# Performance work log

Hardware: AMD Instinct MI355X
Metric: run time of the kernel (lower is better)

The kernel has to match this reference:

```python
import jax, jax.numpy as jnp
import numpy as np

SCALE = 2
PAD = 4
EPS = 1e-5
K = 5
N, C, H, W = 4, 64, 128, 128


def _splits(a, s):
    # (..., W, H) -> (..., W/s, H/s, s*s), block decimation matching torch view/permute
    *lead, Wd, Hd = a.shape
    b = a.reshape(*lead, s, Wd // s, s, Hd // s)
    nl = len(lead)
    b = jnp.transpose(b, tuple(range(nl)) + (nl + 1, nl + 3, nl, nl + 2))
    return b.reshape(*lead, Wd // s, Hd // s, s * s)


def _p2o(psf, Hs, Ws):
    # PSF -> OTF: zero-pad, roll to center at origin, FFT
    kh, kw = psf.shape[-2], psf.shape[-1]
    otf = jnp.zeros(psf.shape[:-2] + (Hs, Ws), psf.dtype).at[..., :kh, :kw].set(psf)
    otf = jnp.roll(otf, (-(kh // 2), -(kw // 2)), axis=(-2, -1))
    return jnp.fft.fftn(otf, axes=(-2, -1))


def _upsample(x, s):
    # s-fold zero-filling upsampler (S^T y)
    n, c, h, w = x.shape
    return jnp.zeros((n, c, h * s, w * s), x.dtype).at[..., ::s, ::s].set(x)


def setup_inputs() -> dict:
    key = jax.random.key(0)
    kx, kw_, _ = jax.random.split(key, 3)
    x = jax.random.normal(kx, (N, C, H, W), dtype=jnp.float32)
    w_raw = jax.random.normal(kw_, (1, C, K, K), dtype=jnp.float32)
    weight = jax.nn.softmax(w_raw.reshape(1, C, -1), axis=-1).reshape(1, C, K, K)
    bias = jnp.zeros((1, C, 1, 1), dtype=jnp.float32)
    return {"x": x, "weight": weight, "bias": bias}


def reference(x, weight, bias):
    s = SCALE
    xp = jnp.pad(x, ((0, 0), (0, 0), (PAD, PAD), (PAD, PAD)), mode="wrap")  # circular
    biaseps = jax.nn.sigmoid(bias - 9.0) + EPS  # (1,C,1,1)
    _, _, h, w = xp.shape
    STy = _upsample(xp, s)  # zero-filled upsample
    # nearest-neighbor interpolate by integer factor s
    xn = jnp.repeat(jnp.repeat(xp, s, axis=-2), s, axis=-1)
    FB = _p2o(weight, h * s, w * s)           # (1,C,hs,ws) complex
    FBC = jnp.conj(FB)
    F2B = jnp.abs(FB) ** 2                     # real
    FBFy = FBC * jnp.fft.fftn(STy, axes=(-2, -1))
    FR = FBFy + jnp.fft.fftn(biaseps * xn, axes=(-2, -1))
    x1 = FB * FR
    FBR = jnp.mean(_splits(x1, s), axis=-1)    # (N,C,h,w) complex
    invW = jnp.mean(_splits(F2B, s), axis=-1)  # (1,C,h,w) real
    invWBR = FBR / (invW + biaseps)
    FCBinvWBR = FBC * jnp.tile(invWBR, (1, 1, s, s))
    FX = (FR - FCBinvWBR) / biaseps
    out = jnp.real(jnp.fft.ifftn(FX, axes=(-2, -1)))
    out = out[..., PAD * s:-PAD * s, PAD * s:-PAD * s]
    return out
```

## Files before the change

kernel.cpp:

```cpp
#include <hip/hip_runtime.h>
#include <math.h>


#define MDIM 136
#define RSCF 146
#define RSC4 73
#define HC   69
#define PLANE_HALF (MDIM*HC)
#define NPLANES 256
#define LDS_BYTES (MDIM*RSC4*16 + 306*8)
#define PI_D 3.14159265358979323846
#define NTH 1024

__device__ __forceinline__ int slot136(int k) { return 17*(k & 7) + (k >> 3); }
__device__ __forceinline__ int slot68(int k)  { return 17*(k & 3) + (k >> 2); }

__device__ __forceinline__ float4 q_add(float4 a, float4 b)
{ return make_float4(a.x+b.x, a.y+b.y, a.z+b.z, a.w+b.w); }
__device__ __forceinline__ float4 q_sub(float4 a, float4 b)
{ return make_float4(a.x-b.x, a.y-b.y, a.z-b.z, a.w-b.w); }
__device__ __forceinline__ float4 q_muli(float4 a, float d)
{ return make_float4(-d*a.y, d*a.x, -d*a.w, d*a.z); }
__device__ __forceinline__ float4 q_scale(float4 a, float s)
{ return make_float4(s*a.x, s*a.y, s*a.z, s*a.w); }
__device__ __forceinline__ float4 q_fma(float4 a, float s, float4 acc)
{ return make_float4(fmaf(a.x,s,acc.x), fmaf(a.y,s,acc.y),
                     fmaf(a.z,s,acc.z), fmaf(a.w,s,acc.w)); }
__device__ __forceinline__ float4 cmul4(float4 q, float2 w)
{ return make_float4(q.x*w.x - q.y*w.y, q.x*w.y + q.y*w.x,
                     q.z*w.x - q.w*w.y, q.z*w.y + q.w*w.x); }

template<int DIR, class F>
__device__ __forceinline__ void dft17_sink(float2* z, int base, int stride, F f)
{
    constexpr float C17[9] = {1.f, 0.93247223f, 0.73900892f, 0.44573836f,
                              0.09226836f, -0.27366299f, -0.60263464f,
                              -0.85021714f, -0.98297310f};
    constexpr float S17[9] = {0.f, 0.36124167f, 0.67369564f, 0.89516329f,
                              0.99573418f, 0.96182564f, 0.79801723f,
                              0.52643216f, 0.18374952f};
    constexpr float d = (DIR > 0) ? 1.f : -1.f;
    float xr[17], xi[17];
#pragma unroll
    for (int n = 0; n < 17; n++) {
        float2 v = z[base + n*stride];
        xr[n] = v.x; xi[n] = v.y;
    }
    float ar[8], ai[8], br[8], bi[8];
#pragma unroll
    for (int n = 1; n <= 8; n++) {
        ar[n-1] = xr[n] + xr[17-n];  ai[n-1] = xi[n] + xi[17-n];
        br[n-1] = xr[n] - xr[17-n];  bi[n-1] = xi[n] - xi[17-n];
    }
    float s0r = xr[0], s0i = xi[0];
#pragma unroll
    for (int n = 0; n < 8; n++) { s0r += ar[n]; s0i += ai[n]; }
    f(0, s0r, s0i);
#pragma unroll
    for (int k = 1; k <= 8; k++) {
        float Pr = xr[0], Pi = xi[0], Qr = 0.f, Qi = 0.f;
#pragma unroll
        for (int n = 1; n <= 8; n++) {
            int m = (k*n) % 17;
            float cc = (m <= 8) ? C17[m] : C17[17-m];
            float ss = (m <= 8) ? S17[m] : -S17[17-m];
            Pr = fmaf(ar[n-1], cc, Pr);
            Pi = fmaf(ai[n-1], cc, Pi);
            Qr = fmaf(br[n-1], ss, Qr);
            Qi = fmaf(bi[n-1], ss, Qi);
        }
        f(k,    Pr - d*Qi, Pi + d*Qr);
        f(17-k, Pr + d*Qi, Pi - d*Qr);
    }
}

template<int DIR>
__device__ __forceinline__ void radix4_tw(float2* z, const float2* t68, int base, int n2,
                                          float2 Z0, float2 Z1, float2 Z2, float2 Z3)
{
    constexpr float d = (DIR > 0) ? 1.0f : -1.0f;
    float t0r = Z0.x+Z2.x, t0i = Z0.y+Z2.y;
    float t1r = Z0.x-Z2.x, t1i = Z0.y-Z2.y;
    float t2r = Z1.x+Z3.x, t2i = Z1.y+Z3.y;
    float t3r = Z1.x-Z3.x, t3i = Z1.y-Z3.y;
    float X0r = t0r+t2r,     X0i = t0i+t2i;
    float X2r = t0r-t2r,     X2i = t0i-t2i;
    float X1r = t1r - d*t3i, X1i = t1i + d*t3r;
    float X3r = t1r + d*t3i, X3i = t1i - d*t3r;
    z[base + n2] = make_float2(X0r, X0i);
    float2 w1 = t68[n2], w2 = t68[17 + n2], w3 = t68[34 + n2];
    if (DIR < 0) { w1.y = -w1.y; w2.y = -w2.y; w3.y = -w3.y; }
    z[base + 17 + n2] = make_float2(X1r*w1.x - X1i*w1.y, X1r*w1.y + X1i*w1.x);
    z[base + 34 + n2] = make_float2(X2r*w2.x - X2i*w2.y, X2r*w2.y + X2i*w2.x);
    z[base + 51 + n2] = make_float2(X3r*w3.x - X3i*w3.y, X3r*w3.y + X3i*w3.x);
}

template<int DIR>
__device__ __forceinline__ void radix4q_tw(float4* z, const float2* t68, int base, int n2,
                                           float4 Z0, float4 Z1, float4 Z2, float4 Z3)
{
    constexpr float d = (DIR > 0) ? 1.0f : -1.0f;
    float4 t0 = q_add(Z0, Z2), t1 = q_sub(Z0, Z2);
    float4 t2 = q_add(Z1, Z3), t3 = q_sub(Z1, Z3);
    float4 X0 = q_add(t0, t2), X2 = q_sub(t0, t2);
    float4 it3 = q_muli(t3, d);
    float4 X1 = q_add(t1, it3), X3 = q_sub(t1, it3);
    z[base + n2] = X0;
    float2 w1 = t68[n2], w2 = t68[17 + n2], w3 = t68[34 + n2];
    z[base + 17 + n2] = cmul4(X1, w1);
    z[base + 34 + n2] = cmul4(X2, w2);
    z[base + 51 + n2] = cmul4(X3, w3);
}

template<int DIR>
__device__ __forceinline__ void fft136_s1_body(float2* z, const float2* t136,
                                               int c, int n2)
{
    constexpr float d = (DIR > 0) ? 1.0f : -1.0f;
    constexpr float C707 = 0.70710678118654752f;
    float xr[8], xi[8];
#pragma unroll
    for (int n1 = 0; n1 < 8; n1++) {
        float2 v = z[(17*n1 + n2)*RSCF + c];
        xr[n1] = v.x; xi[n1] = v.y;
    }
    float e0r = xr[0]+xr[4], e0i = xi[0]+xi[4];
    float e1r = xr[0]-xr[4], e1i = xi[0]-xi[4];
    float o0r = xr[2]+xr[6], o0i = xi[2]+xi[6];
    float o1r = xr[2]-xr[6], o1i = xi[2]-xi[6];
    float E0r = e0r+o0r, E0i = e0i+o0i;
    float E2r = e0r-o0r, E2i = e0i-o0i;
    float E1r = e1r - d*o1i, E1i = e1i + d*o1r;
    float E3r = e1r + d*o1i, E3i = e1i - d*o1r;
    float f0r = xr[1]+xr[5], f0i = xi[1]+xi[5];
    float f1r = xr[1]-xr[5], f1i = xi[1]-xi[5];
    float h0r = xr[3]+xr[7], h0i = xi[3]+xi[7];
    float h1r = xr[3]-xr[7], h1i = xi[3]-xi[7];
    float O0r = f0r+h0r, O0i = f0i+h0i;
    float O2r = f0r-h0r, O2i = f0i-h0i;
    float O1r = f1r - d*h1i, O1i = f1i + d*h1r;
    float O3r = f1r + d*h1i, O3i = f1i - d*h1r;
    float t1r =  C707*(O1r - d*O1i), t1i = C707*(O1i + d*O1r);
    float t2r = -d*O2i,              t2i = d*O2r;
    float t3r = -C707*(O3r + d*O3i), t3i = C707*(d*O3r - O3i);
    float Xr[8], Xi[8];
    Xr[0]=E0r+O0r; Xi[0]=E0i+O0i;  Xr[4]=E0r-O0r; Xi[4]=E0i-O0i;
    Xr[1]=E1r+t1r; Xi[1]=E1i+t1i;  Xr[5]=E1r-t1r; Xi[5]=E1i-t1i;
    Xr[2]=E2r+t2r; Xi[2]=E2i+t2i;  Xr[6]=E2r-t2r; Xi[6]=E2i-t2i;
    Xr[3]=E3r+t3r; Xi[3]=E3i+t3i;  Xr[7]=E3r-t3r; Xi[7]=E3i-t3i;
    z[n2*RSCF + c] = make_float2(Xr[0], Xi[0]);
#pragma unroll
    for (int k1 = 1; k1 < 8; k1++) {
        float2 w = t136[(k1-1)*17 + n2];
        if (DIR < 0) w.y = -w.y;
        z[(17*k1 + n2)*RSCF + c] = make_float2(Xr[k1]*w.x - Xi[k1]*w.y,
                                               Xr[k1]*w.y + Xi[k1]*w.x);
    }
}

template<int DIR>
__device__ __forceinline__ void fft136q_s1_body(float4* z, const float2* t136,
                                                int c, int n2)
{
    constexpr float d = (DIR > 0) ? 1.0f : -1.0f;
    constexpr float C707 = 0.70710678118654752f;
    float4 x[8];
#pragma unroll
    for (int n1 = 0; n1 < 8; n1++) x[n1] = z[(17*n1 + n2)*RSC4 + c];
    float4 e0 = q_add(x[0], x[4]), e1 = q_sub(x[0], x[4]);
    float4 o0 = q_add(x[2], x[6]), o1 = q_sub(x[2], x[6]);
    float4 E0 = q_add(e0, o0), E2 = q_sub(e0, o0);
    float4 io1 = q_muli(o1, d);
    float4 E1 = q_add(e1, io1), E3 = q_sub(e1, io1);
    float4 f0 = q_add(x[1], x[5]), f1 = q_sub(x[1], x[5]);
    float4 h0 = q_add(x[3], x[7]), h1 = q_sub(x[3], x[7]);
    float4 O0 = q_add(f0, h0), O2 = q_sub(f0, h0);
    float4 ih1 = q_muli(h1, d);
    float4 O1 = q_add(f1, ih1), O3 = q_sub(f1, ih1);
    float4 t1 = q_scale(q_add(O1, q_muli(O1, d)), C707);
    float4 t2 = q_muli(O2, d);
    float4 t3 = q_scale(q_sub(O3, q_muli(O3, d)), -C707);
    float4 X0 = q_add(E0, O0), X4 = q_sub(E0, O0);
    float4 X1 = q_add(E1, t1), X5 = q_sub(E1, t1);
    float4 X2 = q_add(E2, t2), X6 = q_sub(E2, t2);
    float4 X3 = q_add(E3, t3), X7 = q_sub(E3, t3);
    z[n2*RSC4 + c] = X0;
    z[(17*1 + n2)*RSC4 + c] = cmul4(X1, t136[0*17 + n2]);
    z[(17*2 + n2)*RSC4 + c] = cmul4(X2, t136[1*17 + n2]);
    z[(17*3 + n2)*RSC4 + c] = cmul4(X3, t136[2*17 + n2]);
    z[(17*4 + n2)*RSC4 + c] = cmul4(X4, t136[3*17 + n2]);
    z[(17*5 + n2)*RSC4 + c] = cmul4(X5, t136[4*17 + n2]);
    z[(17*6 + n2)*RSC4 + c] = cmul4(X6, t136[5*17 + n2]);
    z[(17*7 + n2)*RSC4 + c] = cmul4(X7, t136[6*17 + n2]);
}

__device__ __forceinline__ float4 c2r_pack4(float4 a, float4 b, float2 w)
{
    float Sx = a.x + b.x, Sy = a.y - b.y;
    float Dx = a.x - b.x, Dy = a.y + b.y;
    float Ox = w.x*Dx - w.y*Dy, Oy = w.x*Dy + w.y*Dx;
    float Sz = a.z + b.z, Sw = a.w - b.w;
    float Dz = a.z - b.z, Dw = a.w + b.w;
    float Oz = w.x*Dz - w.y*Dw, Ow = w.x*Dw + w.y*Dz;
    return make_float4(Sx - Oy, Sy + Ox, Sz - Ow, Sw + Oz);
}

__global__ __launch_bounds__(1024, 4) void conv_kernel(const float* __restrict__ x,
                                                       const float4* __restrict__ Abuf,
                                                       float* __restrict__ out)
{
    extern __shared__ float4 z4s[];
    float4* z4    = z4s;
    float2* zf    = (float2*)z4s;
    float2* lutI  = (float2*)(z4s + MDIM*RSC4);
    float2* tI136 = lutI + MDIM;
    float2* tI68  = tI136 + 119;
    const int tid = threadIdx.x;
    const int nc  = blockIdx.x;
    const int c   = nc & 63;

    if (tid < MDIM) {
        float s, cc; sincosf(2.0f*(float)PI_D*(float)tid/136.0f, &s, &cc);
        lutI[tid] = make_float2(cc, s);
    } else if (tid < MDIM + 119) {
        int it = tid - MDIM;
        int k1 = it/17 + 1, n2 = it - (it/17)*17;
        float s, cc; sincosf((float)(PI_D/68.0)*(float)(k1*n2), &s, &cc);
        tI136[it] = make_float2(cc, s);
    } else if (tid < MDIM + 119 + 51) {
        int it = tid - MDIM - 119;
        int j = it/17, n2 = it - 17*j;
        float s, cc; sincosf((float)(PI_D/34.0)*(float)((j+1)*n2), &s, &cc);
        tI68[it] = make_float2(cc, s);
    }
    const float* xp = x + (size_t)nc * (128*128);
    {
        int i = tid / 68, n = tid - (tid/68)*68;
        for (int e = tid; e < MDIM*68; e += NTH) {
            int si = (i + 124) & 127;
            int j0 = (2*n + 124) & 127;
            zf[i*RSCF + n] = *reinterpret_cast<const float2*>(xp + si*128 + j0);
            i += 15; n += 4; if (n >= 68) { n -= 68; i++; }
        }
    }
    __syncthreads();
    {
        int row = tid / 17;
        int n2  = tid - row*17;
        for (int e = tid; e < MDIM*17; e += NTH) {
            int base = row*RSCF;
            float2 Z0 = zf[base + n2];
            float2 Z1 = zf[base + 17 + n2];
            float2 Z2 = zf[base + 34 + n2];
            float2 Z3 = zf[base + 51 + n2];
            radix4_tw<-1>(zf, tI68, base, n2, Z0, Z1, Z2, Z3);
            row += 60; n2 += 4; if (n2 >= 17) { n2 -= 17; row++; }
        }
    }
    __syncthreads();
    if (tid < MDIM*4) {
        int row = tid >> 2, k1 = tid & 3;
        int base = row*RSCF + 17*k1;
        dft17_sink<-1>(zf, base, 1, [&](int k2, float re, float im) {
            zf[base + k2] = make_float2(re, im);
        });
    }
    __syncthreads();
    {
        int row = tid / 35, k = tid - (tid/35)*35;
        for (int e = tid; e < MDIM*35; e += NTH) {
            int base = row*RSCF;
            int sa = slot68(k);
            float2 Za = zf[base+sa];
            float Zar = Za.x, Zai = Za.y;
            float Zbr, Zbi; int sb;
            if (k == 0) { Zbr = Zar; Zbi = Zai; sb = 68; }
            else {
                int kk = 68-k; sb = slot68(kk);
                float2 Zb = zf[base+sb]; Zbr = Zb.x; Zbi = Zb.y;
            }
            float2 w = lutI[k];
            float wc = w.x, ws = -w.y;
            float Er = 0.5f*(Zar + Zbr), Ei = 0.5f*(Zai - Zbi);
            float Dr = 0.5f*(Zar - Zbr), Di = 0.5f*(Zai + Zbi);
            float Tr = wc*Dr - ws*Di, Ti = wc*Di + ws*Dr;
            zf[base+sa] = make_float2(Er + Ti, Ei - Tr);
            float E2r = Er,  E2i = -Ei;
            float D2r = -Dr, D2i = Di;
            float w2c = -wc, w2s = ws;
            float T2r = w2c*D2r - w2s*D2i, T2i = w2c*D2i + w2s*D2r;
            zf[base+sb] = make_float2(E2r + T2i, E2i - T2r);
            row += 29; k += 9; if (k >= 35) { k -= 35; row++; }
        }
    }
    __syncthreads();
    for (int e = tid; e < HC*17; e += NTH) {
        int cc = (e*241) >> 12;
        int n2 = e - cc*17;
        fft136_s1_body<-1>(zf, tI136, cc, n2);
    }
    __syncthreads();
    if (tid < HC*8) {
        int cc = tid >> 3, k1 = tid & 7;
        int base = 17*k1*RSCF + cc;
        dft17_sink<-1>(zf, base, RSCF, [&](int k2, float re, float im) {
            zf[base + k2*RSCF] = make_float2(re, im);
        });
    }
    __syncthreads();
    float2 Xreg[10];
    {
        int g1 = tid / HC, g2 = tid - (tid/HC)*HC;
#pragma unroll
        for (int k = 0; k < 10; k++) {
            if (k < 9 || tid < PLANE_HALF - 9*NTH) {
                int cq = (g2 == 68) ? 68 : slot68(g2);
                Xreg[k] = zf[slot136(g1)*RSCF + cq];
            }
            g1 += 14; g2 += 58; if (g2 >= HC) { g2 -= HC; g1++; }
        }
    }
    __syncthreads();
    float* op = out + (size_t)nc * (256*256);
#pragma unroll 1
    for (int u = 0; u < 2; u++) {
        const float4* Ap = Abuf + (size_t)(c*2 + u) * PLANE_HALF;
        {
            int g1 = tid / HC, g2 = tid - (tid/HC)*HC;
#pragma unroll
            for (int k = 0; k < 10; k++) {
                if (k < 9 || tid < PLANE_HALF - 9*NTH) {
                    float2 xv = Xreg[k];
                    float4 av = Ap[tid + k*NTH];
                    z4[g1*RSC4 + g2] = make_float4(
                        av.x*xv.x - av.y*xv.y, av.x*xv.y + av.y*xv.x,
                        av.z*xv.x - av.w*xv.y, av.z*xv.y + av.w*xv.x);
                }
                g1 += 14; g2 += 58; if (g2 >= HC) { g2 -= HC; g1++; }
            }
        }
        __syncthreads();
        for (int e = tid; e < HC*17; e += NTH) {
            int cc = (e*241) >> 12;
            int n2 = e - cc*17;
            fft136q_s1_body<1>(z4, tI136, cc, n2);
        }
        __syncthreads();
        {
            float2* z2 = (float2*)z4;
            for (int it = tid; it < 2*HC*8; it += NTH) {
                int half = it & 1;
                int i  = it >> 1;
                int cc = i >> 3, k1 = i & 7;
                int base = 2*(17*k1*RSC4 + cc) + half;
                dft17_sink<1>(z2, base, 2*RSC4, [&](int k2, float re, float im) {
                    z2[base + k2*2*RSC4] = make_float2(re, im);
                });
            }
        }
        __syncthreads();
        for (int it = tid; it < MDIM*9; it += NTH) {
            int row = (it*7282) >> 16;
            int g   = it - row*9;
            int base = row*RSC4;
            if (g == 0) {
                float4 T0  = z4[base],    T17 = z4[base+17], T34 = z4[base+34],
                       T51 = z4[base+51], T68 = z4[base+68];
                float4 Z0 = c2r_pack4(T0,  T68, lutI[0]);
                float4 Z1 = c2r_pack4(T17, T51, lutI[17]);
                float4 Z2 = c2r_pack4(T34, T34, lutI[34]);
                float4 Z3 = c2r_pack4(T51, T17, lutI[51]);
                radix4q_tw<1>(z4, tI68, base, 0, Z0, Z1, Z2, Z3);
            } else {
                int gb = 17 - g;
                float4 Ta0 = z4[base+g],    Ta1 = z4[base+g+17],
                       Ta2 = z4[base+g+34], Ta3 = z4[base+g+51];
                float4 Tb0 = z4[base+gb],    Tb1 = z4[base+gb+17],
                       Tb2 = z4[base+gb+34], Tb3 = z4[base+gb+51];
                float4 Za0 = c2r_pack4(Ta0, Tb3, lutI[g]);
                float4 Za1 = c2r_pack4(Ta1, Tb2, lutI[g+17]);
                float4 Za2 = c2r_pack4(Ta2, Tb1, lutI[g+34]);
                float4 Za3 = c2r_pack4(Ta3, Tb0, lutI[g+51]);
                float4 Zb0 = c2r_pack4(Tb0, Ta3, lutI[gb]);
                float4 Zb1 = c2r_pack4(Tb1, Ta2, lutI[gb+17]);
                float4 Zb2 = c2r_pack4(Tb2, Ta1, lutI[gb+34]);
                float4 Zb3 = c2r_pack4(Tb3, Ta0, lutI[gb+51]);
                radix4q_tw<1>(z4, tI68, base, g,  Za0, Za1, Za2, Za3);
                radix4q_tw<1>(z4, tI68, base, gb, Zb0, Zb1, Zb2, Zb3);
            }
        }
        __syncthreads();
        {
            float2* z2 = (float2*)z4;
            for (int it = tid; it < 2*MDIM*4; it += NTH) {
                int half = it & 1;
                int i   = it >> 1;
                int row = i >> 2, k1 = i & 3;
                int base = 2*(row*RSC4 + 17*k1) + half;
                dft17_sink<1>(z2, base, 2, [&](int k2, float re, float im) {
                    z2[base + 2*k2] = make_float2(re, im);
                });
            }
        }
        __syncthreads();
        {
            int m  = 2 + (tid & 63);
            int y1 = 4 + (tid >> 6);
            int a  = slot136(y1)*RSC4 + slot68(m);
            float* rowp = op + (size_t)(2*y1 + u - 8)*256 + 4*m - 8;
#pragma unroll
            for (int it = 0; it < 8; ++it) {
                float4 w = z4[a];
                *reinterpret_cast<float4*>(rowp) = make_float4(w.x, w.z, w.y, w.w);
                a += 2*RSC4;
                rowp += 32*256;
            }
        }
        __syncthreads();
    }
}

__global__ void prep_kernel(const float* __restrict__ weight,
                            const float* __restrict__ bias,
                            float4* __restrict__ Abuf)
{
    __shared__ float tabc[272], tabs[272];
    __shared__ float Rs[69*5*4];
    for (int t = threadIdx.x; t < 272; t += blockDim.x) {
        float s, c; sincosf(-2.0f*(float)PI_D*(float)t/272.0f, &s, &c);
        tabc[t] = c; tabs[t] = s;
    }
    const int c     = blockIdx.x >> 3;
    const int chunk = blockIdx.x & 7;
    const float* wp = weight + c*25;
    const float r = 1.0f/(1.0f + expf(9.0f - bias[c])) + 1e-5f;
    __syncthreads();
    for (int it = threadIdx.x; it < 69*5; it += blockDim.x) {
        int g2 = it / 5, a = it - 5*g2;
        float c2 = tabc[g2], s2 = tabs[g2];
        float e2r[5], e2i[5];
        e2r[2]=1.0f; e2i[2]=0.0f; e2r[3]=c2; e2i[3]=s2;
        e2r[4]=c2*c2-s2*s2; e2i[4]=2.0f*c2*s2;
        e2r[1]=c2; e2i[1]=-s2; e2r[0]=e2r[4]; e2i[0]=-e2i[4];
        float w0=wp[a*5+0], w1=wp[a*5+1], w2=wp[a*5+2], w3=wp[a*5+3], w4=wp[a*5+4];
        float Rer = w0*e2r[0] + w2*e2r[2] + w4*e2r[4];
        float Rei = w0*e2i[0] + w2*e2i[2] + w4*e2i[4];
        float Ror = w1*e2r[1] + w3*e2r[3];
        float Roi = w1*e2i[1] + w3*e2i[3];
        Rs[it*4+0] = Rer + Ror;  Rs[it*4+1] = Rei + Roi;
        Rs[it*4+2] = Rer - Ror;  Rs[it*4+3] = Rei - Roi;
    }
    __syncthreads();

    const int e_lo = chunk * 1173;
    const int e_hi = e_lo + 1173;
    int e  = e_lo + (int)threadIdx.x;
    int g1 = e / HC, g2 = e - (e/HC)*HC;
    for (; e < e_hi; e += blockDim.x) {
        float c1 = tabc[g1], s1 = tabs[g1];
        float e1r[5], e1i[5];
        e1r[2]=1.0f; e1i[2]=0.0f; e1r[3]=c1; e1i[3]=s1;
        e1r[4]=c1*c1-s1*s1; e1i[4]=2.0f*c1*s1;
        e1r[1]=c1; e1i[1]=-s1; e1r[0]=e1r[4]; e1i[0]=-e1i[4];

        float FBr[2][2], FBi[2][2];
#pragma unroll
        for (int b1 = 0; b1 < 2; b1++) {
            float Per=0.f, Pei=0.f, Por=0.f, Poi=0.f;
#pragma unroll
            for (int a = 0; a < 5; a++) {
                float Rr = Rs[(g2*5+a)*4 + 2*b1];
                float Ri = Rs[(g2*5+a)*4 + 2*b1 + 1];
                float tr = e1r[a]*Rr - e1i[a]*Ri;
                float ti = e1r[a]*Ri + e1i[a]*Rr;
                if (a & 1) { Por += tr; Poi += ti; } else { Per += tr; Pei += ti; }
            }
            FBr[0][b1] = Per + Por;  FBi[0][b1] = Pei + Poi;
            FBr[1][b1] = Per - Por;  FBi[1][b1] = Pei - Poi;
        }
        float c2 = tabc[g2], s2 = tabs[g2];
        float ur[2]={1.0f+c1, 1.0f-c1}, ui[2]={s1, -s1};
        float vr[2]={1.0f+c2, 1.0f-c2}, vi[2]={s2, -s2};
        float Br_[2][2], Bi_[2][2];
#pragma unroll
        for (int a1 = 0; a1 < 2; a1++)
#pragma unroll
            for (int b1 = 0; b1 < 2; b1++) {
                Br_[a1][b1] = ur[a1]*vr[b1] - ui[a1]*vi[b1];
                Bi_[a1][b1] = ur[a1]*vi[b1] + ui[a1]*vr[b1];
            }
        float invW=0.f, Qr=0.f, Qi=0.f;
#pragma unroll
        for (int a1 = 0; a1 < 2; a1++)
#pragma unroll
            for (int b1 = 0; b1 < 2; b1++) {
                invW += FBr[a1][b1]*FBr[a1][b1] + FBi[a1][b1]*FBi[a1][b1];
                Qr += FBr[a1][b1]*Br_[a1][b1] - FBi[a1][b1]*Bi_[a1][b1];
                Qi += FBr[a1][b1]*Bi_[a1][b1] + FBi[a1][b1]*Br_[a1][b1];
            }
        invW *= 0.25f; Qr *= 0.25f; Qi *= 0.25f;
        float den = 1.0f/(invW + r);
        float Sr = (1.0f - Qr)*den, Si = -Qi*den;
        float Mr[2][2], Mi[2][2];
#pragma unroll
        for (int a1 = 0; a1 < 2; a1++)
#pragma unroll
            for (int b1 = 0; b1 < 2; b1++) {
                Mr[a1][b1] = Br_[a1][b1] + FBr[a1][b1]*Sr + FBi[a1][b1]*Si;
                Mi[a1][b1] = Bi_[a1][b1] + FBr[a1][b1]*Si - FBi[a1][b1]*Sr;
            }
        const float scale = 1.0f/73984.0f;
#pragma unroll
        for (int uu = 0; uu < 2; uu++) {
            float ov[4];
#pragma unroll
            for (int vv = 0; vv < 2; vv++) {
                float sr=0.f, si=0.f;
#pragma unroll
                for (int a1 = 0; a1 < 2; a1++)
#pragma unroll
                    for (int b1 = 0; b1 < 2; b1++) {
                        if ((a1*uu + b1*vv) & 1) { sr -= Mr[a1][b1]; si -= Mi[a1][b1]; }
                        else                     { sr += Mr[a1][b1]; si += Mi[a1][b1]; }
                    }
                int t = g1*uu + g2*vv;
                float pc = tabc[t], ps = -tabs[t];
                ov[2*vv]   = (pc*sr - ps*si)*scale;
                ov[2*vv+1] = (pc*si + ps*sr)*scale;
            }
            Abuf[((size_t)(c*2 + uu))*PLANE_HALF + e] =
                make_float4(ov[0], ov[1], ov[2], ov[3]);
        }
        g1 += 3; g2 += 49; if (g2 >= HC) { g2 -= HC; g1++; }
    }
}

extern "C" void kernel_launch(void* const* d_in, const int* in_sizes, int n_in,
                              void* d_out, int out_size, void* d_ws, size_t ws_size,
                              hipStream_t stream)
{
    const float* x      = (const float*)d_in[0];
    const float* weight = (const float*)d_in[1];
    const float* bias   = (const float*)d_in[2];
    float* out = (float*)d_out;

    float4* Abuf = (float4*)d_ws;

    (void)hipFuncSetAttribute((const void*)conv_kernel,
                              hipFuncAttributeMaxDynamicSharedMemorySize,
                              (int)LDS_BYTES);

    prep_kernel<<<512, 256, 0, stream>>>(weight, bias, Abuf);
    conv_kernel<<<NPLANES, 1024, LDS_BYTES, stream>>>(x, Abuf, out);
}
```

Before: 131.0 us.

## Process one output phase per inverse FFT pass to halve LDS footprint

The inverse-FFT loop now handles each of the four (u,v) output phases separately with float2 planes, where it used to handle two phases at once as float4. Twiddle and LUT tables move into the padding columns of the LDS matrix, so LDS per block shrinks to about half and launch bounds ask for higher occupancy. The cost is twice as many inverse-FFT passes, barriers and Abuf reads, plus scattered scalar output stores where the code used float4 stores.

```diff
diff --git a/kernel.cpp b/kernel.cpp
--- a/kernel.cpp
+++ b/kernel.cpp
@@ -3,32 +3,23 @@
 
 
 #define MDIM 136
-#define RSCF 146
-#define RSC4 73
+#define RSC2 73
 #define HC   69
 #define PLANE_HALF (MDIM*HC)
 #define NPLANES 256
-#define LDS_BYTES (MDIM*RSC4*16 + 306*8)
+#define LDS_BYTES (MDIM*RSC2*8)
 #define PI_D 3.14159265358979323846
 #define NTH 1024
 
 __device__ __forceinline__ int slot136(int k) { return 17*(k & 7) + (k >> 3); }
 __device__ __forceinline__ int slot68(int k)  { return 17*(k & 3) + (k >> 2); }
 
-__device__ __forceinline__ float4 q_add(float4 a, float4 b)
-{ return make_float4(a.x+b.x, a.y+b.y, a.z+b.z, a.w+b.w); }
-__device__ __forceinline__ float4 q_sub(float4 a, float4 b)
-{ return make_float4(a.x-b.x, a.y-b.y, a.z-b.z, a.w-b.w); }
-__device__ __forceinline__ float4 q_muli(float4 a, float d)
-{ return make_float4(-d*a.y, d*a.x, -d*a.w, d*a.z); }
-__device__ __forceinline__ float4 q_scale(float4 a, float s)
-{ return make_float4(s*a.x, s*a.y, s*a.z, s*a.w); }
-__device__ __forceinline__ float4 q_fma(float4 a, float s, float4 acc)
-{ return make_float4(fmaf(a.x,s,acc.x), fmaf(a.y,s,acc.y),
-                     fmaf(a.z,s,acc.z), fmaf(a.w,s,acc.w)); }
-__device__ __forceinline__ float4 cmul4(float4 q, float2 w)
-{ return make_float4(q.x*w.x - q.y*w.y, q.x*w.y + q.y*w.x,
-                     q.z*w.x - q.w*w.y, q.z*w.y + q.w*w.x); }
+__device__ __forceinline__ float2 LUTI(const float2* z, int t)
+{ return z[t*RSC2 + 69]; }
+__device__ __forceinline__ float2 T136(const float2* z, int i)
+{ return z[i*RSC2 + 70]; }
+__device__ __forceinline__ float2 T68v(const float2* z, int i)
+{ return z[i*RSC2 + 71]; }
 
 template<int DIR, class F>
 __device__ __forceinline__ void dft17_sink(float2* z, int base, int stride, F f)
@@ -75,7 +66,7 @@
 }
 
 template<int DIR>
-__device__ __forceinline__ void radix4_tw(float2* z, const float2* t68, int base, int n2,
+__device__ __forceinline__ void radix4_tw(float2* z, int base, int n2,
                                           float2 Z0, float2 Z1, float2 Z2, float2 Z3)
 {
     constexpr float d = (DIR > 0) ? 1.0f : -1.0f;
@@ -88,7 +79,7 @@
     float X1r = t1r - d*t3i, X1i = t1i + d*t3r;
     float X3r = t1r + d*t3i, X3i = t1i - d*t3r;
     z[base + n2] = make_float2(X0r, X0i);
-    float2 w1 = t68[n2], w2 = t68[17 + n2], w3 = t68[34 + n2];
+    float2 w1 = T68v(z, n2), w2 = T68v(z, 17 + n2), w3 = T68v(z, 34 + n2);
     if (DIR < 0) { w1.y = -w1.y; w2.y = -w2.y; w3.y = -w3.y; }
     z[base + 17 + n2] = make_float2(X1r*w1.x - X1i*w1.y, X1r*w1.y + X1i*w1.x);
     z[base + 34 + n2] = make_float2(X2r*w2.x - X2i*w2.y, X2r*w2.y + X2i*w2.x);
@@ -96,32 +87,14 @@
 }
 
 template<int DIR>
-__device__ __forceinline__ void radix4q_tw(float4* z, const float2* t68, int base, int n2,
-                                           float4 Z0, float4 Z1, float4 Z2, float4 Z3)
-{
-    constexpr float d = (DIR > 0) ? 1.0f : -1.0f;
-    float4 t0 = q_add(Z0, Z2), t1 = q_sub(Z0, Z2);
-    float4 t2 = q_add(Z1, Z3), t3 = q_sub(Z1, Z3);
-    float4 X0 = q_add(t0, t2), X2 = q_sub(t0, t2);
-    float4 it3 = q_muli(t3, d);
-    float4 X1 = q_add(t1, it3), X3 = q_sub(t1, it3);
-    z[base + n2] = X0;
-    float2 w1 = t68[n2], w2 = t68[17 + n2], w3 = t68[34 + n2];
-    z[base + 17 + n2] = cmul4(X1, w1);
-    z[base + 34 + n2] = cmul4(X2, w2);
-    z[base + 51 + n2] = cmul4(X3, w3);
-}
-
-template<int DIR>
-__device__ __forceinline__ void fft136_s1_body(float2* z, const float2* t136,
-                                               int c, int n2)
+__device__ __forceinline__ void fft136_s1_body(float2* z, int c, int n2)
 {
     constexpr float d = (DIR > 0) ? 1.0f : -1.0f;
     constexpr float C707 = 0.70710678118654752f;
     float xr[8], xi[8];
 #pragma unroll
     for (int n1 = 0; n1 < 8; n1++) {
-        float2 v = z[(17*n1 + n2)*RSCF + c];
+        float2 v = z[(17*n1 + n2)*RSC2 + c];
         xr[n1] = v.x; xi[n1] = v.y;
     }
     float e0r = xr[0]+xr[4], e0i = xi[0]+xi[4];
@@ -148,90 +121,46 @@
     Xr[1]=E1r+t1r; Xi[1]=E1i+t1i;  Xr[5]=E1r-t1r; Xi[5]=E1i-t1i;
     Xr[2]=E2r+t2r; Xi[2]=E2i+t2i;  Xr[6]=E2r-t2r; Xi[6]=E2i-t2i;
     Xr[3]=E3r+t3r; Xi[3]=E3i+t3i;  Xr[7]=E3r-t3r; Xi[7]=E3i-t3i;
-    z[n2*RSCF + c] = make_float2(Xr[0], Xi[0]);
+    z[n2*RSC2 + c] = make_float2(Xr[0], Xi[0]);
 #pragma unroll
     for (int k1 = 1; k1 < 8; k1++) {
-        float2 w = t136[(k1-1)*17 + n2];
+        float2 w = T136(z, (k1-1)*17 + n2);
         if (DIR < 0) w.y = -w.y;
-        z[(17*k1 + n2)*RSCF + c] = make_float2(Xr[k1]*w.x - Xi[k1]*w.y,
+        z[(17*k1 + n2)*RSC2 + c] = make_float2(Xr[k1]*w.x - Xi[k1]*w.y,
                                                Xr[k1]*w.y + Xi[k1]*w.x);
     }
 }
 
-template<int DIR>
-__device__ __forceinline__ void fft136q_s1_body(float4* z, const float2* t136,
-                                                int c, int n2)
-{
-    constexpr float d = (DIR > 0) ? 1.0f : -1.0f;
-    constexpr float C707 = 0.70710678118654752f;
-    float4 x[8];
-#pragma unroll
-    for (int n1 = 0; n1 < 8; n1++) x[n1] = z[(17*n1 + n2)*RSC4 + c];
-    float4 e0 = q_add(x[0], x[4]), e1 = q_sub(x[0], x[4]);
-    float4 o0 = q_add(x[2], x[6]), o1 = q_sub(x[2], x[6]);
-    float4 E0 = q_add(e0, o0), E2 = q_sub(e0, o0);
-    float4 io1 = q_muli(o1, d);
-    float4 E1 = q_add(e1, io1), E3 = q_sub(e1, io1);
-    float4 f0 = q_add(x[1], x[5]), f1 = q_sub(x[1], x[5]);
-    float4 h0 = q_add(x[3], x[7]), h1 = q_sub(x[3], x[7]);
-    float4 O0 = q_add(f0, h0), O2 = q_sub(f0, h0);
-    float4 ih1 = q_muli(h1, d);
-    float4 O1 = q_add(f1, ih1), O3 = q_sub(f1, ih1);
-    float4 t1 = q_scale(q_add(O1, q_muli(O1, d)), C707);
-    float4 t2 = q_muli(O2, d);
-    float4 t3 = q_scale(q_sub(O3, q_muli(O3, d)), -C707);
-    float4 X0 = q_add(E0, O0), X4 = q_sub(E0, O0);
-    float4 X1 = q_add(E1, t1), X5 = q_sub(E1, t1);
-    float4 X2 = q_add(E2, t2), X6 = q_sub(E2, t2);
-    float4 X3 = q_add(E3, t3), X7 = q_sub(E3, t3);
-    z[n2*RSC4 + c] = X0;
-    z[(17*1 + n2)*RSC4 + c] = cmul4(X1, t136[0*17 + n2]);
-    z[(17*2 + n2)*RSC4 + c] = cmul4(X2, t136[1*17 + n2]);
-    z[(17*3 + n2)*RSC4 + c] = cmul4(X3, t136[2*17 + n2]);
-    z[(17*4 + n2)*RSC4 + c] = cmul4(X4, t136[3*17 + n2]);
-    z[(17*5 + n2)*RSC4 + c] = cmul4(X5, t136[4*17 + n2]);
-    z[(17*6 + n2)*RSC4 + c] = cmul4(X6, t136[5*17 + n2]);
-    z[(17*7 + n2)*RSC4 + c] = cmul4(X7, t136[6*17 + n2]);
-}
-
-__device__ __forceinline__ float4 c2r_pack4(float4 a, float4 b, float2 w)
-{
-    float Sx = a.x + b.x, Sy = a.y - b.y;
-    float Dx = a.x - b.x, Dy = a.y + b.y;
-    float Ox = w.x*Dx - w.y*Dy, Oy = w.x*Dy + w.y*Dx;
-    float Sz = a.z + b.z, Sw = a.w - b.w;
-    float Dz = a.z - b.z, Dw = a.w + b.w;
-    float Oz = w.x*Dz - w.y*Dw, Ow = w.x*Dw + w.y*Dz;
-    return make_float4(Sx - Oy, Sy + Ox, Sz - Ow, Sw + Oz);
-}
-
-__global__ __launch_bounds__(1024, 4) void conv_kernel(const float* __restrict__ x,
-                                                       const float4* __restrict__ Abuf,
+__device__ __forceinline__ float2 c2r_pack(float2 a, float2 b, float2 w)
+{
+    float Sr = a.x + b.x, Si = a.y - b.y;
+    float Dr = a.x - b.x, Di = a.y + b.y;
+    float Or = w.x*Dr - w.y*Di, Oi = w.x*Di + w.y*Dr;
+    return make_float2(Sr - Oi, Si + Or);
+}
+
+__global__ __launch_bounds__(1024, 8) void conv_kernel(const float* __restrict__ x,
+                                                       const float2* __restrict__ Abuf,
                                                        float* __restrict__ out)
 {
-    extern __shared__ float4 z4s[];
-    float4* z4    = z4s;
-    float2* zf    = (float2*)z4s;
-    float2* lutI  = (float2*)(z4s + MDIM*RSC4);
-    float2* tI136 = lutI + MDIM;
-    float2* tI68  = tI136 + 119;
+    extern __shared__ float2 z2[];
     const int tid = threadIdx.x;
     const int nc  = blockIdx.x;
     const int c   = nc & 63;
 
     if (tid < MDIM) {
         float s, cc; sincosf(2.0f*(float)PI_D*(float)tid/136.0f, &s, &cc);
-        lutI[tid] = make_float2(cc, s);
+        z2[tid*RSC2 + 69] = make_float2(cc, s);
     } else if (tid < MDIM + 119) {
         int it = tid - MDIM;
         int k1 = it/17 + 1, n2 = it - (it/17)*17;
         float s, cc; sincosf((float)(PI_D/68.0)*(float)(k1*n2), &s, &cc);
-        tI136[it] = make_float2(cc, s);
+        z2[it*RSC2 + 70] = make_float2(cc, s);
     } else if (tid < MDIM + 119 + 51) {
         int it = tid - MDIM - 119;
         int j = it/17, n2 = it - 17*j;
         float s, cc; sincosf((float)(PI_D/34.0)*(float)((j+1)*n2), &s, &cc);
-        tI68[it] = make_float2(cc, s);
+        z2[it*RSC2 + 71] = make_float2(cc, s);
     }
     const float* xp = x + (size_t)nc * (128*128);
     {
@@ -239,7 +168,7 @@
         for (int e = tid; e < MDIM*68; e += NTH) {
             int si = (i + 124) & 127;
             int j0 = (2*n + 124) & 127;
-            zf[i*RSCF + n] = *reinterpret_cast<const float2*>(xp + si*128 + j0);
+            z2[i*RSC2 + n] = *reinterpret_cast<const float2*>(xp + si*128 + j0);
             i += 15; n += 4; if (n >= 68) { n -= 68; i++; }
         }
     }
@@ -248,48 +177,48 @@
         int row = tid / 17;
         int n2  = tid - row*17;
         for (int e = tid; e < MDIM*17; e += NTH) {
-            int base = row*RSCF;
-            float2 Z0 = zf[base + n2];
-            float2 Z1 = zf[base + 17 + n2];
-            float2 Z2 = zf[base + 34 + n2];
-            float2 Z3 = zf[base + 51 + n2];
-            radix4_tw<-1>(zf, tI68, base, n2, Z0, Z1, Z2, Z3);
+            int base = row*RSC2;
+            float2 Z0 = z2[base + n2];
+            float2 Z1 = z2[base + 17 + n2];
+            float2 Z2 = z2[base + 34 + n2];
+            float2 Z3 = z2[base + 51 + n2];
+            radix4_tw<-1>(z2, base, n2, Z0, Z1, Z2, Z3);
             row += 60; n2 += 4; if (n2 >= 17) { n2 -= 17; row++; }
         }
     }
     __syncthreads();
     if (tid < MDIM*4) {
         int row = tid >> 2, k1 = tid & 3;
-        int base = row*RSCF + 17*k1;
-        dft17_sink<-1>(zf, base, 1, [&](int k2, float re, float im) {
-            zf[base + k2] = make_float2(re, im);
+        int base = row*RSC2 + 17*k1;
+        dft17_sink<-1>(z2, base, 1, [&](int k2, float re, float im) {
+            z2[base + k2] = make_float2(re, im);
         });
     }
     __syncthreads();
     {
         int row = tid / 35, k = tid - (tid/35)*35;
         for (int e = tid; e < MDIM*35; e += NTH) {
-            int base = row*RSCF;
+            int base = row*RSC2;
             int sa = slot68(k);
-            float2 Za = zf[base+sa];
+            float2 Za = z2[base+sa];
             float Zar = Za.x, Zai = Za.y;
             float Zbr, Zbi; int sb;
             if (k == 0) { Zbr = Zar; Zbi = Zai; sb = 68; }
             else {
                 int kk = 68-k; sb = slot68(kk);
-                float2 Zb = zf[base+sb]; Zbr = Zb.x; Zbi = Zb.y;
-            }
-            float2 w = lutI[k];
+                float2 Zb = z2[base+sb]; Zbr = Zb.x; Zbi = Zb.y;
+            }
+            float2 w = LUTI(z2, k);
             float wc = w.x, ws = -w.y;
             float Er = 0.5f*(Zar + Zbr), Ei = 0.5f*(Zai - Zbi);
             float Dr = 0.5f*(Zar - Zbr), Di = 0.5f*(Zai + Zbi);
             float Tr = wc*Dr - ws*Di, Ti = wc*Di + ws*Dr;
-            zf[base+sa] = make_float2(Er + Ti, Ei - Tr);
+            z2[base+sa] = make_float2(Er + Ti, Ei - Tr);
             float E2r = Er,  E2i = -Ei;
             float D2r = -Dr, D2i = Di;
             float w2c = -wc, w2s = ws;
             float T2r = w2c*D2r - w2s*D2i, T2i = w2c*D2i + w2s*D2r;
-            zf[base+sb] = make_float2(E2r + T2i, E2i - T2r);
+            z2[base+sb] = make_float2(E2r + T2i, E2i - T2r);
             row += 29; k += 9; if (k >= 35) { k -= 35; row++; }
         }
     }
@@ -297,14 +226,14 @@
     for (int e = tid; e < HC*17; e += NTH) {
         int cc = (e*241) >> 12;
         int n2 = e - cc*17;
-        fft136_s1_body<-1>(zf, tI136, cc, n2);
+        fft136_s1_body<-1>(z2, cc, n2);
     }
     __syncthreads();
     if (tid < HC*8) {
         int cc = tid >> 3, k1 = tid & 7;
-        int base = 17*k1*RSCF + cc;
-        dft17_sink<-1>(zf, base, RSCF, [&](int k2, float re, float im) {
-            zf[base + k2*RSCF] = make_float2(re, im);
+        int base = 17*k1*RSC2 + cc;
+        dft17_sink<-1>(z2, base, RSC2, [&](int k2, float re, float im) {
+            z2[base + k2*RSC2] = make_float2(re, im);
         });
     }
     __syncthreads();
@@ -315,7 +244,7 @@
         for (int k = 0; k < 10; k++) {
             if (k < 9 || tid < PLANE_HALF - 9*NTH) {
                 int cq = (g2 == 68) ? 68 : slot68(g2);
-                Xreg[k] = zf[slot136(g1)*RSCF + cq];
+                Xreg[k] = z2[slot136(g1)*RSC2 + cq];
             }
             g1 += 14; g2 += 58; if (g2 >= HC) { g2 -= HC; g1++; }
         }
@@ -323,18 +252,18 @@
     __syncthreads();
     float* op = out + (size_t)nc * (256*256);
 #pragma unroll 1
-    for (int u = 0; u < 2; u++) {
-        const float4* Ap = Abuf + (size_t)(c*2 + u) * PLANE_HALF;
+    for (int uv = 0; uv < 4; uv++) {
+        const int u = uv >> 1, v = uv & 1;
+        const float2* Ap = Abuf + (size_t)(c*4 + u*2 + v) * PLANE_HALF;
         {
             int g1 = tid / HC, g2 = tid - (tid/HC)*HC;
 #pragma unroll
             for (int k = 0; k < 10; k++) {
                 if (k < 9 || tid < PLANE_HALF - 9*NTH) {
                     float2 xv = Xreg[k];
-                    float4 av = Ap[tid + k*NTH];
-                    z4[g1*RSC4 + g2] = make_float4(
-                        av.x*xv.x - av.y*xv.y, av.x*xv.y + av.y*xv.x,
-                        av.z*xv.x - av.w*xv.y, av.z*xv.y + av.w*xv.x);
+                    float2 av = Ap[tid + k*NTH];
+                    z2[g1*RSC2 + g2] = make_float2(av.x*xv.x - av.y*xv.y,
+                                                   av.x*xv.y + av.y*xv.x);
                 }
                 g1 += 14; g2 += 58; if (g2 >= HC) { g2 -= HC; g1++; }
             }
@@ -343,76 +272,67 @@
         for (int e = tid; e < HC*17; e += NTH) {
             int cc = (e*241) >> 12;
             int n2 = e - cc*17;
-            fft136q_s1_body<1>(z4, tI136, cc, n2);
-        }
-        __syncthreads();
-        {
-            float2* z2 = (float2*)z4;
-            for (int it = tid; it < 2*HC*8; it += NTH) {
-                int half = it & 1;
-                int i  = it >> 1;
-                int cc = i >> 3, k1 = i & 7;
-                int base = 2*(17*k1*RSC4 + cc) + half;
-                dft17_sink<1>(z2, base, 2*RSC4, [&](int k2, float re, float im) {
-                    z2[base + k2*2*RSC4] = make_float2(re, im);
-                });
-            }
+            fft136_s1_body<1>(z2, cc, n2);
+        }
+        __syncthreads();
+        if (tid < HC*8) {
+            int cc = tid >> 3, k1 = tid & 7;
+            int base = 17*k1*RSC2 + cc;
+            dft17_sink<1>(z2, base, RSC2, [&](int k2, float re, float im) {
+                z2[base + k2*RSC2] = make_float2(re, im);
+            });
         }
         __syncthreads();
         for (int it = tid; it < MDIM*9; it += NTH) {
             int row = (it*7282) >> 16;
             int g   = it - row*9;
-            int base = row*RSC4;
+            int base = row*RSC2;
             if (g == 0) {
-                float4 T0  = z4[base],    T17 = z4[base+17], T34 = z4[base+34],
-                       T51 = z4[base+51], T68 = z4[base+68];
-                float4 Z0 = c2r_pack4(T0,  T68, lutI[0]);
-                float4 Z1 = c2r_pack4(T17, T51, lutI[17]);
-                float4 Z2 = c2r_pack4(T34, T34, lutI[34]);
-                float4 Z3 = c2r_pack4(T51, T17, lutI[51]);
-                radix4q_tw<1>(z4, tI68, base, 0, Z0, Z1, Z2, Z3);
+                float2 T0  = z2[base],    T17 = z2[base+17], T34 = z2[base+34],
+                       T51 = z2[base+51], T68 = z2[base+68];
+                float2 Z0 = c2r_pack(T0,  T68, LUTI(z2, 0));
+                float2 Z1 = c2r_pack(T17, T51, LUTI(z2, 17));
+                float2 Z2 = c2r_pack(T34, T34, LUTI(z2, 34));
+                float2 Z3 = c2r_pack(T51, T17, LUTI(z2, 51));
+                radix4_tw<1>(z2, base, 0, Z0, Z1, Z2, Z3);
             } else {
                 int gb = 17 - g;
-                float4 Ta0 = z4[base+g],    Ta1 = z4[base+g+17],
-                       Ta2 = z4[base+g+34], Ta3 = z4[base+g+51];
-                float4 Tb0 = z4[base+gb],    Tb1 = z4[base+gb+17],
-                       Tb2 = z4[base+gb+34], Tb3 = z4[base+gb+51];
-                float4 Za0 = c2r_pack4(Ta0, Tb3, lutI[g]);
-                float4 Za1 = c2r_pack4(Ta1, Tb2, lutI[g+17]);
-                float4 Za2 = c2r_pack4(Ta2, Tb1, lutI[g+34]);
-                float4 Za3 = c2r_pack4(Ta3, Tb0, lutI[g+51]);
-                float4 Zb0 = c2r_pack4(Tb0, Ta3, lutI[gb]);
-                float4 Zb1 = c2r_pack4(Tb1, Ta2, lutI[gb+17]);
-                float4 Zb2 = c2r_pack4(Tb2, Ta1, lutI[gb+34]);
-                float4 Zb3 = c2r_pack4(Tb3, Ta0, lutI[gb+51]);
-                radix4q_tw<1>(z4, tI68, base, g,  Za0, Za1, Za2, Za3);
-                radix4q_tw<1>(z4, tI68, base, gb, Zb0, Zb1, Zb2, Zb3);
-            }
-        }
-        __syncthreads();
-        {
-            float2* z2 = (float2*)z4;
-            for (int it = tid; it < 2*MDIM*4; it += NTH) {
-                int half = it & 1;
-                int i   = it >> 1;
-                int row = i >> 2, k1 = i & 3;
-                int base = 2*(row*RSC4 + 17*k1) + half;
-                dft17_sink<1>(z2, base, 2, [&](int k2, float re, float im) {
-                    z2[base + 2*k2] = make_float2(re, im);
-                });
-            }
+                float2 Ta0 = z2[base+g],    Ta1 = z2[base+g+17],
+                       Ta2 = z2[base+g+34], Ta3 = z2[base+g+51];
+                float2 Tb0 = z2[base+gb],    Tb1 = z2[base+gb+17],
+                       Tb2 = z2[base+gb+34], Tb3 = z2[base+gb+51];
+                float2 Za0 = c2r_pack(Ta0, Tb3, LUTI(z2, g));
+                float2 Za1 = c2r_pack(Ta1, Tb2, LUTI(z2, g+17));
+                float2 Za2 = c2r_pack(Ta2, Tb1, LUTI(z2, g+34));
+                float2 Za3 = c2r_pack(Ta3, Tb0, LUTI(z2, g+51));
+                float2 Zb0 = c2r_pack(Tb0, Ta3, LUTI(z2, gb));
+                float2 Zb1 = c2r_pack(Tb1, Ta2, LUTI(z2, gb+17));
+                float2 Zb2 = c2r_pack(Tb2, Ta1, LUTI(z2, gb+34));
+                float2 Zb3 = c2r_pack(Tb3, Ta0, LUTI(z2, gb+51));
+                radix4_tw<1>(z2, base, g,  Za0, Za1, Za2, Za3);
+                radix4_tw<1>(z2, base, gb, Zb0, Zb1, Zb2, Zb3);
+            }
+        }
+        __syncthreads();
+        if (tid < MDIM*4) {
+            int row = tid >> 2, k1 = tid & 3;
+            int base = row*RSC2 + 17*k1;
+            dft17_sink<1>(z2, base, 1, [&](int k2, float re, float im) {
+                z2[base + k2] = make_float2(re, im);
+            });
         }
         __syncthreads();
         {
             int m  = 2 + (tid & 63);
             int y1 = 4 + (tid >> 6);
-            int a  = slot136(y1)*RSC4 + slot68(m);
-            float* rowp = op + (size_t)(2*y1 + u - 8)*256 + 4*m - 8;
+            int a  = slot136(y1)*RSC2 + slot68(m);
+            float* rowp = op + (size_t)(2*y1 + u - 8)*256 + 4*m + v - 8;
 #pragma unroll
             for (int it = 0; it < 8; ++it) {
-                float4 w = z4[a];
-                *reinterpret_cast<float4*>(rowp) = make_float4(w.x, w.z, w.y, w.w);
-                a += 2*RSC4;
+                float2 w = z2[a];
+                rowp[0] = w.x;
+                rowp[2] = w.y;
+                a += 2*RSC2;
                 rowp += 32*256;
             }
         }
@@ -422,7 +342,7 @@
 
 __global__ void prep_kernel(const float* __restrict__ weight,
                             const float* __restrict__ bias,
-                            float4* __restrict__ Abuf)
+                            float2* __restrict__ Abuf)
 {
     __shared__ float tabc[272], tabs[272];
     __shared__ float Rs[69*5*4];
@@ -511,8 +431,7 @@
             }
         const float scale = 1.0f/73984.0f;
 #pragma unroll
-        for (int uu = 0; uu < 2; uu++) {
-            float ov[4];
+        for (int uu = 0; uu < 2; uu++)
 #pragma unroll
             for (int vv = 0; vv < 2; vv++) {
                 float sr=0.f, si=0.f;
@@ -525,12 +444,9 @@
                     }
                 int t = g1*uu + g2*vv;
                 float pc = tabc[t], ps = -tabs[t];
-                ov[2*vv]   = (pc*sr - ps*si)*scale;
-                ov[2*vv+1] = (pc*si + ps*sr)*scale;
-            }
-            Abuf[((size_t)(c*2 + uu))*PLANE_HALF + e] =
-                make_float4(ov[0], ov[1], ov[2], ov[3]);
-        }
+                Abuf[((size_t)(c*4 + uu*2 + vv))*PLANE_HALF + e] =
+                    make_float2((pc*sr - ps*si)*scale, (pc*si + ps*sr)*scale);
+            }
         g1 += 3; g2 += 49; if (g2 >= HC) { g2 -= HC; g1++; }
     }
 }
@@ -544,7 +460,7 @@
     const float* bias   = (const float*)d_in[2];
     float* out = (float*)d_out;
 
-    float4* Abuf = (float4*)d_ws;
+    float2* Abuf = (float2*)d_ws;
 
     (void)hipFuncSetAttribute((const void*)conv_kernel,
                               hipFuncAttributeMaxDynamicSharedMemorySize,
```

Result: slower. 186.8 us (+42.7%).
